# Optimization experiments

Measured on AMD Instinct MI355X. Metric: run time of the kernel, lower is better.

The kernel has to match this reference:

```python
import jax, jax.numpy as jnp
import numpy as np

N_USER, N_ITEM = 60000, 60000
N = N_USER + N_ITEM
E_BASE = 1500000
P = 200000
IN_DIM, HID, OUT = 128, 128, 64
K_MAX = 0.5


def setup_inputs() -> dict:
    key = jax.random.key(0)
    ks = jax.random.split(key, 20)
    feat_user = jax.random.normal(ks[0], (N_USER, 256), jnp.float32)
    feat_item = jax.random.normal(ks[1], (N_ITEM, 128), jnp.float32)
    src_b = jax.random.randint(ks[2], (E_BASE,), 0, N, jnp.int32)
    dst_b = jax.random.randint(ks[3], (E_BASE,), 0, N, jnp.int32)
    loops = jnp.arange(N, dtype=jnp.int32)  # dgl.add_self_loop
    src = jnp.concatenate([src_b, loops])
    dst = jnp.concatenate([dst_b, loops])
    pos_src = jax.random.randint(ks[4], (P,), 0, N, jnp.int32)
    pos_dst = jax.random.randint(ks[5], (P,), 0, N, jnp.int32)
    neg_src = jax.random.randint(ks[6], (P,), 0, N, jnp.int32)
    neg_dst = jax.random.randint(ks[7], (P,), 0, N, jnp.int32)
    s = 0.05
    W_user = jax.random.normal(ks[8], (256, IN_DIM), jnp.float32) * s
    b_user = jnp.zeros((IN_DIM,), jnp.float32)
    W_item = jax.random.normal(ks[9], (128, IN_DIM), jnp.float32) * s
    b_item = jnp.zeros((IN_DIM,), jnp.float32)
    W_gat = jax.random.normal(ks[10], (IN_DIM, HID), jnp.float32) * s
    attn_l = jax.random.normal(ks[11], (HID,), jnp.float32) * s
    attn_r = jax.random.normal(ks[12], (HID,), jnp.float32) * s
    gat_bias = jnp.zeros((HID,), jnp.float32)
    W_pred = jax.random.normal(ks[13], (HID, OUT), jnp.float32) * s
    b_pred = jnp.zeros((OUT,), jnp.float32)
    return {
        "feat_user": feat_user, "feat_item": feat_item,
        "W_user": W_user, "b_user": b_user, "W_item": W_item, "b_item": b_item,
        "W_gat": W_gat, "attn_l": attn_l, "attn_r": attn_r, "gat_bias": gat_bias,
        "W_pred": W_pred, "b_pred": b_pred,
        "src": src, "dst": dst,
        "pos_src": pos_src, "pos_dst": pos_dst,
        "neg_src": neg_src, "neg_dst": neg_dst,
        "alpha_T": 1,
    }


def _gat_conv(x, src, dst, W_gat, attn_l, attn_r, gat_bias):
    # DGL GATConv, 1 head: fc (no bias), additive attention, edge softmax over dst.
    z = x @ W_gat                              # [N, HID]
    el = z @ attn_l                            # [N]
    er = z @ attn_r                            # [N]
    e = jax.nn.leaky_relu(el[src] + er[dst], 0.2)   # [E]
    m = jax.ops.segment_max(e, dst, num_segments=N)  # per-dst max (self loops -> no empty segs)
    ex = jnp.exp(e - m[dst])
    ssum = jax.ops.segment_sum(ex, dst, num_segments=N)
    a = ex / ssum[dst]                          # edge softmax coeffs
    msg = z[src] * a[:, None]                   # [E, HID]
    out = jax.ops.segment_sum(msg, dst, num_segments=N) + gat_bias
    return jax.nn.elu(out)                      # activation=F.elu


def _hold_loss(score, k_T):
    l = jax.nn.log_sigmoid(score)
    hold = k_T * jnp.max(l)
    l = jnp.where(l > hold, 0.0, l)
    return -jnp.sum(l)


def reference(feat_user, feat_item, W_user, b_user, W_item, b_item,
              W_gat, attn_l, attn_r, gat_bias, W_pred, b_pred,
              src, dst, pos_src, pos_dst, neg_src, neg_dst, alpha_T):
    # per-type input projection then concat in ntype order (dgl.to_homogeneous)
    hu = feat_user @ W_user + b_user
    hi = feat_item @ W_item + b_item
    x = jnp.concatenate([hu, hi], axis=0)       # [N, IN_DIM]
    h = _gat_conv(x, src, dst, W_gat, attn_l, attn_r, gat_bias)
    pos_score = jnp.sum(h[pos_src] * h[pos_dst], axis=1)
    neg_score = jnp.sum(h[neg_src] * h[neg_dst], axis=1)
    k_T = K_MAX if K_MAX <= alpha_T else alpha_T   # k_T = min(k_max, alpha_T)
    loss = _hold_loss(pos_score, k_T) + _hold_loss(neg_score, k_T)
    out = h[:N_USER] @ W_pred + b_pred          # predict_type 'user' == type id 0
    return loss, out
```

## Files before the change

### kernel.cpp

```cpp
#include <hip/hip_runtime.h>
#include <hip/hip_bf16.h>
#include <math.h>

#define NUSER 60000
#define NITEM 60000
#define NNODE 120000
#define BSH 9
#define NB 235
#define CAP 8192

typedef __attribute__((ext_vector_type(8))) short bf16x8;
typedef __attribute__((ext_vector_type(4))) float f32x4;
typedef __attribute__((ext_vector_type(2))) float f32x2;
typedef __attribute__((ext_vector_type(4))) unsigned short u16x4;

__device__ __forceinline__ float leaky02(float x) { return x > 0.f ? x : 0.2f * x; }

__device__ __forceinline__ float inv_ord(unsigned int u) {
  unsigned int bits = (u & 0x80000000u) ? (u & 0x7FFFFFFFu) : ~u;
  return __uint_as_float(bits);
}
__device__ __forceinline__ unsigned int ord_of(float f) {
  unsigned int u = __float_as_uint(f);
  return (u & 0x80000000u) ? ~u : (u | 0x80000000u);
}
__device__ __forceinline__ short f2bs(float f) {
  __hip_bfloat16 h = __float2bfloat16(f);
  return *reinterpret_cast<short*>(&h);
}

__device__ __forceinline__ void f8fma(f32x2& acc, float w, unsigned int u) {
  f32x2 zz = __builtin_amdgcn_cvt_pk_f32_fp8(u, false);
  f32x2 ww; ww.x = w; ww.y = w;
  acc = __builtin_elementwise_fma(ww, zz, acc);
}
__device__ __forceinline__ void fp8dot(f32x2& acc, unsigned int ua, unsigned int ub) {
  f32x2 a0 = __builtin_amdgcn_cvt_pk_f32_fp8(ua, false);
  f32x2 a1 = __builtin_amdgcn_cvt_pk_f32_fp8(ua, true);
  f32x2 b0 = __builtin_amdgcn_cvt_pk_f32_fp8(ub, false);
  f32x2 b1 = __builtin_amdgcn_cvt_pk_f32_fp8(ub, true);
  acc = __builtin_elementwise_fma(a0, b0, acc);
  acc = __builtin_elementwise_fma(a1, b1, acc);
}

__global__ __launch_bounds__(256) void prep_count_kernel(
    const float* __restrict__ Wu, const float* __restrict__ bu, const float* __restrict__ Wi,
    const float* __restrict__ bi, const float* __restrict__ Wg, const float* __restrict__ Wp,
    __hip_bfloat16* __restrict__ Bp_u, __hip_bfloat16* __restrict__ Bp_i,
    __hip_bfloat16* __restrict__ Bp_p, float* __restrict__ bf_u, float* __restrict__ bf_i,
    const int* __restrict__ dst, int* __restrict__ btotal, int E) {
  __shared__ int cnt[NB];
  if (blockIdx.x < 512) {
    int bid = blockIdx.x;
    for (int t = threadIdx.x; t < NB; t += 256) cnt[t] = 0;
    __syncthreads();
    for (int i = bid * 256 + threadIdx.x; i < E; i += 512 * 256)
      atomicAdd(&cnt[dst[i] >> BSH], 1);
    __syncthreads();
    for (int t = threadIdx.x; t < NB; t += 256)
      if (cnt[t]) atomicAdd(&btotal[t], cnt[t]);
    return;
  }
  int t = (blockIdx.x - 512) * 256 + threadIdx.x;
  if (t < 32768) {
    int j = t & 7, lane = (t >> 3) & 63, rest = t >> 9;
    int nt = rest & 7, ks = rest >> 3;
    int k = ks * 32 + ((lane >> 4) << 3) + j;
    int n = nt * 16 + (lane & 15);
    float acc = 0.f;
#pragma unroll 8
    for (int jj = 0; jj < 128; ++jj) acc = fmaf(Wu[k * 128 + jj], Wg[jj * 128 + n], acc);
    Bp_u[t] = __float2bfloat16(acc);
  } else if (t < 49152) {
    int tt = t - 32768;
    int j = tt & 7, lane = (tt >> 3) & 63, rest = tt >> 9;
    int nt = rest & 7, ks = rest >> 3;
    int k = ks * 32 + ((lane >> 4) << 3) + j;
    int n = nt * 16 + (lane & 15);
    float acc = 0.f;
#pragma unroll 8
    for (int jj = 0; jj < 128; ++jj) acc = fmaf(Wi[k * 128 + jj], Wg[jj * 128 + n], acc);
    Bp_i[tt] = __float2bfloat16(acc);
  } else if (t < 57344) {
    int tt = t - 49152;
    int j = tt & 7, lane = (tt >> 3) & 63, rest = tt >> 9;
    int nt = rest & 3, ks = rest >> 2;
    int k = ks * 32 + ((lane >> 4) << 3) + j;
    int n = nt * 16 + (lane & 15);
    Bp_p[tt] = __float2bfloat16(Wp[k * 64 + n]);
  } else if (t < 57344 + 256) {
    int n = t - 57344;
    if (n < 128) {
      float acc = 0.f;
      for (int jj = 0; jj < 128; ++jj) acc = fmaf(bu[jj], Wg[jj * 128 + n], acc);
      bf_u[n] = acc;
    } else {
      int nn = n - 128;
      float acc = 0.f;
      for (int jj = 0; jj < 128; ++jj) acc = fmaf(bi[jj], Wg[jj * 128 + nn], acc);
      bf_i[nn] = acc;
    }
  }
}

__global__ void bscan_kernel(const int* __restrict__ btotal, int* __restrict__ bstart,
                             int* __restrict__ gcur) {
  __shared__ int s[256];
  int t = threadIdx.x;
  int v = (t < NB) ? btotal[t] : 0;
  s[t] = v;
  __syncthreads();
  for (int off = 1; off < 256; off <<= 1) {
    int a = (t >= off) ? s[t - off] : 0;
    __syncthreads();
    s[t] += a;
    __syncthreads();
  }
  int excl = s[t] - v;
  if (t < NB) { bstart[t] = excl; gcur[t] = excl; }
  if (t == NB - 1) bstart[NB] = s[t];
}

template <int K>
__device__ __forceinline__ void zgemm_body(
    char* smem, const float* __restrict__ A, const __hip_bfloat16* __restrict__ Bp,
    const float* __restrict__ bias, const float* __restrict__ al, const float* __restrict__ ar,
    unsigned char* __restrict__ z8, float* __restrict__ el, float* __restrict__ er, int M,
    int blk) {
  float(*lds)[140] = (float(*)[140])smem;
  const int lane = threadIdx.x & 63, wv = threadIdx.x >> 6;
  const int t = threadIdx.x;
  const int C4 = K / 4;
  for (int f = t; f < 64 * C4; f += 256) {
    int row = f / C4, c4 = f - row * C4;
    int grow = blk * 64 + row;
    if (grow >= M) grow = M - 1;
    float4 a = *(const float4*)(A + (size_t)grow * K + c4 * 4);
    u16x4 pk;
    pk[0] = (unsigned short)f2bs(a.x);
    pk[1] = (unsigned short)f2bs(a.y);
    pk[2] = (unsigned short)f2bs(a.z);
    pk[3] = (unsigned short)f2bs(a.w);
    unsigned int byte = (unsigned int)row * (K * 2) + (unsigned int)c4 * 8;
    byte ^= (row & 7) << 4;
    *(u16x4*)(smem + byte) = pk;
  }
  __syncthreads();
  const bf16x8* bp = (const bf16x8*)Bp;
  const int frow = wv * 16 + (lane & 15);
  f32x4 acc[8] = {};
#pragma unroll
  for (int ks = 0; ks < K / 32; ++ks) {
    unsigned int byte = (unsigned int)frow * (K * 2) + (unsigned int)(ks * 32 + ((lane >> 4) << 3)) * 2;
    byte ^= (frow & 7) << 4;
    bf16x8 af = *(const bf16x8*)(smem + byte);
#pragma unroll
    for (int nt = 0; nt < 8; ++nt) {
      bf16x8 bfr = bp[(ks * 8 + nt) * 64 + lane];
      acc[nt] = __builtin_amdgcn_mfma_f32_16x16x32_bf16(af, bfr, acc[nt], 0, 0, 0);
    }
  }
  __syncthreads();
#pragma unroll
  for (int nt = 0; nt < 8; ++nt) {
    float b = bias[nt * 16 + (lane & 15)];
#pragma unroll
    for (int r = 0; r < 4; ++r)
      lds[wv * 16 + (lane >> 4) * 4 + r][nt * 16 + (lane & 15)] = acc[nt][r] + b;
  }
  __syncthreads();
  int row = threadIdx.x >> 2;
  int q = threadIdx.x & 3;
  int gm = blk * 64 + row;
  float pl = 0.f, pr = 0.f;
  if (gm < M) {
    const float* lrow = &lds[row][q * 32];
#pragma unroll
    for (int v4 = 0; v4 < 4; ++v4) {
      float f[8];
#pragma unroll
      for (int j = 0; j < 8; ++j) {
        f[j] = lrow[v4 * 8 + j];
        int c = q * 32 + v4 * 8 + j;
        pl = fmaf(f[j], al[c], pl);
        pr = fmaf(f[j], ar[c], pr);
      }
      unsigned int w0 = (unsigned int)__builtin_amdgcn_cvt_pk_fp8_f32(f[0], f[1], 0, false);
      w0 = (unsigned int)__builtin_amdgcn_cvt_pk_fp8_f32(f[2], f[3], (int)w0, true);
      unsigned int w1 = (unsigned int)__builtin_amdgcn_cvt_pk_fp8_f32(f[4], f[5], 0, false);
      w1 = (unsigned int)__builtin_amdgcn_cvt_pk_fp8_f32(f[6], f[7], (int)w1, true);
      uint2 st; st.x = w0; st.y = w1;
      *(uint2*)(z8 + (size_t)gm * 128 + q * 32 + v4 * 8) = st;
    }
  }
  pl += __shfl_xor(pl, 1, 64); pl += __shfl_xor(pl, 2, 64);
  pr += __shfl_xor(pr, 1, 64); pr += __shfl_xor(pr, 2, 64);
  if (q == 0 && gm < M) { el[gm] = pl; er[gm] = pr; }
}

__global__ __launch_bounds__(256) void zgemm_scatter_kernel(
    const float* __restrict__ Au, const __hip_bfloat16* __restrict__ Bpu,
    const float* __restrict__ bfu, const float* __restrict__ Ai,
    const __hip_bfloat16* __restrict__ Bpi, const float* __restrict__ bfi,
    const float* __restrict__ al, const float* __restrict__ ar, unsigned char* __restrict__ z8,
    float* __restrict__ el, float* __restrict__ er, int SC, int GU,
    const int* __restrict__ src, const int* __restrict__ dst, int* __restrict__ gcur,
    unsigned int* __restrict__ scratch, int E) {
  __shared__ __align__(16) char smem[64 * 140 * 4];
  int bx = blockIdx.x;
  if (bx < SC) {
    int* cnt = (int*)smem;
    int* basep = cnt + NB;
    for (int t = threadIdx.x; t < NB; t += 256) cnt[t] = 0;
    __syncthreads();
    const int i0 = bx * 4096;
    unsigned int v_[16];
    int b_[16], r_[16];
#pragma unroll
    for (int j = 0; j < 16; ++j) {
      int i = i0 + j * 256 + threadIdx.x;
      b_[j] = -1;
      if (i < E) {
        int d = dst[i];
        int s = src[i];
        int b = d >> BSH;
        b_[j] = b;
        r_[j] = atomicAdd(&cnt[b], 1);
        v_[j] = (unsigned int)s | ((unsigned int)(d & 511) << 17);
      }
    }
    __syncthreads();
    for (int t = threadIdx.x; t < NB; t += 256)
      basep[t] = cnt[t] ? atomicAdd(&gcur[t], cnt[t]) : 0;
    __syncthreads();
#pragma unroll
    for (int j = 0; j < 16; ++j)
      if (b_[j] >= 0) scratch[basep[b_[j]] + r_[j]] = v_[j];
    return;
  }
  int gb = bx - SC;
  if (gb < GU)
    zgemm_body<256>(smem, Au, Bpu, bfu, al, ar, z8, el, er, NUSER, gb);
  else
    zgemm_body<128>(smem, Ai, Bpi, bfi, al, ar, z8 + (size_t)NUSER * 128, el + NUSER, er + NUSER,
                    NITEM, gb - GU);
}

__global__ __launch_bounds__(512) void bsort_kernel(const unsigned int* __restrict__ scratch,
                                                    const int* __restrict__ bstart,
                                                    int* __restrict__ offs, int* __restrict__ ssrc) {
  __shared__ unsigned int buf[CAP];
  __shared__ int cnt[512], scn[512], cur[512];
  int b = blockIdx.x, t = threadIdx.x;
  int s = bstart[b], e = bstart[b + 1], n = e - s;
  int d0 = b << BSH;
  int ndst = NNODE - d0;
  if (ndst > 512) ndst = 512;
  cnt[t] = 0;
  cur[t] = 0;
  __syncthreads();
  bool fit = (n <= CAP);
  if (fit) {
    for (int i = t; i < n; i += 512) {
      unsigned int v = scratch[s + i];
      buf[i] = v;
      atomicAdd(&cnt[v >> 17], 1);
    }
  } else {
    for (int i = t; i < n; i += 512) atomicAdd(&cnt[scratch[s + i] >> 17], 1);
  }
  __syncthreads();
  scn[t] = cnt[t];
  __syncthreads();
  for (int off = 1; off < 512; off <<= 1) {
    int a = (t >= off) ? scn[t - off] : 0;
    __syncthreads();
    scn[t] += a;
    __syncthreads();
  }
  int start = scn[t] - cnt[t];
  if (t < ndst) offs[d0 + t] = s + start;
  if (b == NB - 1 && t == 0) offs[NNODE] = e;
  __syncthreads();
  cnt[t] = start;
  __syncthreads();
  if (fit) {
    for (int i = t; i < n; i += 512) {
      unsigned int v = buf[i];
      int dl = v >> 17;
      int r = atomicAdd(&cur[dl], 1);
      ssrc[s + cnt[dl] + r] = (int)(v & 0x1FFFFu);
    }
  } else {
    for (int i = t; i < n; i += 512) {
      unsigned int v = scratch[s + i];
      int dl = v >> 17;
      int r = atomicAdd(&cur[dl], 1);
      ssrc[s + cnt[dl] + r] = (int)(v & 0x1FFFFu);
    }
  }
}

__global__ __launch_bounds__(256) void aggregate_kernel(
    const unsigned char* __restrict__ z8, const float* __restrict__ el,
    const float* __restrict__ er, const int* __restrict__ offs, const int* __restrict__ ssrc,
    const float* __restrict__ gat_bias, __hip_bfloat16* __restrict__ h,
    unsigned char* __restrict__ h8) {
  __shared__ __align__(16) float2 ew[4][128];
  int wv = threadIdx.x >> 6, lane = threadIdx.x & 63;
  int d = blockIdx.x * 4 + wv;
  int s0 = offs[d], s1 = offs[d + 1];
  int deg = s1 - s0;
  float erd = er[d];
  const unsigned short* zw = (const unsigned short*)z8;
  f32x2 acc = {0.f, 0.f};
  float ssum = 0.f;
  if (deg <= 128) {
    float w0 = 0.f, w1 = 0.f;
    int o0 = 0, o1 = 0;
    if (lane < deg) { int s = ssrc[s0 + lane]; o0 = s << 6; w0 = __expf(leaky02(el[s] + erd)); }
    if (64 + lane < deg) { int s = ssrc[s0 + 64 + lane]; o1 = s << 6; w1 = __expf(leaky02(el[s] + erd)); }
    ew[wv][lane] = make_float2(w0, __int_as_float(o0));
    ew[wv][64 + lane] = make_float2(w1, __int_as_float(o1));
    __builtin_amdgcn_wave_barrier();
    int i = 0;
    for (; i + 8 <= deg; i += 8) {
      float4 p0 = *(const float4*)&ew[wv][i];
      float4 p1 = *(const float4*)&ew[wv][i + 2];
      float4 p2 = *(const float4*)&ew[wv][i + 4];
      float4 p3 = *(const float4*)&ew[wv][i + 6];
      unsigned int u0 = zw[__float_as_uint(p0.y) + lane];
      unsigned int u1 = zw[__float_as_uint(p0.w) + lane];
      unsigned int u2 = zw[__float_as_uint(p1.y) + lane];
      unsigned int u3 = zw[__float_as_uint(p1.w) + lane];
      unsigned int u4 = zw[__float_as_uint(p2.y) + lane];
      unsigned int u5 = zw[__float_as_uint(p2.w) + lane];
      unsigned int u6 = zw[__float_as_uint(p3.y) + lane];
      unsigned int u7 = zw[__float_as_uint(p3.w) + lane];
      ssum += ((p0.x + p0.z) + (p1.x + p1.z)) + ((p2.x + p2.z) + (p3.x + p3.z));
      f8fma(acc, p0.x, u0); f8fma(acc, p0.z, u1);
      f8fma(acc, p1.x, u2); f8fma(acc, p1.z, u3);
      f8fma(acc, p2.x, u4); f8fma(acc, p2.z, u5);
      f8fma(acc, p3.x, u6); f8fma(acc, p3.z, u7);
    }
    for (; i + 2 <= deg; i += 2) {
      float4 p = *(const float4*)&ew[wv][i];
      unsigned int ua = zw[__float_as_uint(p.y) + lane];
      unsigned int ub = zw[__float_as_uint(p.w) + lane];
      ssum += p.x + p.z;
      f8fma(acc, p.x, ua); f8fma(acc, p.z, ub);
    }
    if (i < deg) {
      float2 pp = ew[wv][i];
      unsigned int u = zw[__float_as_uint(pp.y) + lane];
      ssum += pp.x;
      f8fma(acc, pp.x, u);
    }
  } else {
    for (int i2 = s0; i2 < s1; ++i2) {
      int s = ssrc[i2];
      float w = __expf(leaky02(el[s] + erd));
      ssum += w;
      unsigned int u = zw[((unsigned int)s << 6) + lane];
      f8fma(acc, w, u);
    }
  }
  float inv = 1.f / ssum;
  float o0f = acc.x * inv + gat_bias[lane * 2];
  float o1f = acc.y * inv + gat_bias[lane * 2 + 1];
  o0f = (o0f > 0.f) ? o0f : (__expf(o0f) - 1.f);
  o1f = (o1f > 0.f) ? o1f : (__expf(o1f) - 1.f);
  ushort2 ov;
  ov.x = (unsigned short)((unsigned int)f2bs(o0f) & 0xFFFFu);
  ov.y = (unsigned short)((unsigned int)f2bs(o1f) & 0xFFFFu);
  *(ushort2*)((unsigned short*)h + (size_t)d * 128 + lane * 2) = ov;
  int pk8 = __builtin_amdgcn_cvt_pk_fp8_f32(o0f, o1f, 0, false);
  *(unsigned short*)(h8 + (size_t)d * 128 + lane * 2) = (unsigned short)(pk8 & 0xFFFF);
}

__global__ __launch_bounds__(256) void scorepred_kernel(
    const unsigned char* __restrict__ h8, const int* __restrict__ ps, const int* __restrict__ pd,
    const int* __restrict__ ns, const int* __restrict__ nd, float* __restrict__ l_pos,
    float* __restrict__ l_neg, unsigned int* __restrict__ maxacc, int P,
    const __hip_bfloat16* __restrict__ h, const __hip_bfloat16* __restrict__ Bp,
    const float* __restrict__ bias, float* __restrict__ outp, int GP, int NSB) {
  if ((int)blockIdx.x < GP) {
    const int lane = threadIdx.x & 63, wv = threadIdx.x >> 6;
    const int m0 = blockIdx.x * 64 + wv * 16;
    int arow = m0 + (lane & 15);
    if (arow >= NUSER) arow = NUSER - 1;
    const bf16x8* a0 = (const bf16x8*)(h + (size_t)arow * 128) + (lane >> 4);
    const bf16x8* bp = (const bf16x8*)Bp;
    f32x4 acc[4] = {};
#pragma unroll
    for (int ks = 0; ks < 4; ++ks) {
      bf16x8 af = a0[ks * 4];
#pragma unroll
      for (int nt = 0; nt < 4; ++nt) {
        bf16x8 bfr = bp[(ks * 4 + nt) * 64 + lane];
        acc[nt] = __builtin_amdgcn_mfma_f32_16x16x32_bf16(af, bfr, acc[nt], 0, 0, 0);
      }
    }
#pragma unroll
    for (int nt = 0; nt < 4; ++nt) {
      int col = nt * 16 + (lane & 15);
      float b = bias[col];
#pragma unroll
      for (int r = 0; r < 4; ++r) {
        int m = m0 + (lane >> 4) * 4 + r;
        if (m < NUSER) outp[(size_t)m * 64 + col] = acc[nt][r] + b;
      }
    }
    return;
  }
  const int sb = blockIdx.x - GP;
  const int g16 = threadIdx.x >> 4, l16 = threadIdx.x & 15;
  const uint2* h2 = (const uint2*)h8;
  const int stride = NSB * 16;
  const int tot = 2 * P;
  float mpos = -1e30f, mneg = -1e30f;

  int i = sb * 16 + g16;
  int aC = 0, bC = 0;
  if (i < tot) {
    bool n = i >= P; int j = n ? i - P : i;
    aC = n ? ns[j] : ps[j]; bC = n ? nd[j] : pd[j];
  }
  uint2 vaC = {0, 0}, vbC = {0, 0};
  if (i < tot) {
    vaC = h2[(size_t)aC * 16 + l16];
    vbC = h2[(size_t)bC * 16 + l16];
  }
  int i1 = i + stride;
  int aN = 0, bN = 0;
  if (i1 < tot) {
    bool n = i1 >= P; int j = n ? i1 - P : i1;
    aN = n ? ns[j] : ps[j]; bN = n ? nd[j] : pd[j];
  }

  while (i < tot) {
    uint2 vaN = {0, 0}, vbN = {0, 0};
    if (i1 < tot) {
      vaN = h2[(size_t)aN * 16 + l16];
      vbN = h2[(size_t)bN * 16 + l16];
    }
    int i2 = i1 + stride;
    int aN2 = 0, bN2 = 0;
    if (i2 < tot) {
      bool n = i2 >= P; int j = n ? i2 - P : i2;
      aN2 = n ? ns[j] : ps[j]; bN2 = n ? nd[j] : pd[j];
    }
    f32x2 acc = {0.f, 0.f};
    fp8dot(acc, vaC.x, vbC.x);
    fp8dot(acc, vaC.y, vbC.y);
    float s = acc.x + acc.y;
    s += __shfl_xor(s, 1, 16);
    s += __shfl_xor(s, 2, 16);
    s += __shfl_xor(s, 4, 16);
    s += __shfl_xor(s, 8, 16);
    float lv = fminf(s, 0.f) - log1pf(__expf(-fabsf(s)));
    bool neg = i >= P;
    int j = neg ? i - P : i;
    if (l16 == 0) (neg ? l_neg : l_pos)[j] = lv;
    if (neg) mneg = fmaxf(mneg, lv); else mpos = fmaxf(mpos, lv);
    i = i1; i1 = i2;
    aC = aN; bC = bN; aN = aN2; bN = bN2;
    vaC = vaN; vbC = vbN;
  }
  __shared__ float red0[256], red1[256];
  red0[threadIdx.x] = mpos;
  red1[threadIdx.x] = mneg;
  __syncthreads();
  for (int off = 128; off; off >>= 1) {
    if (threadIdx.x < off) {
      red0[threadIdx.x] = fmaxf(red0[threadIdx.x], red0[threadIdx.x + off]);
      red1[threadIdx.x] = fmaxf(red1[threadIdx.x], red1[threadIdx.x + off]);
    }
    __syncthreads();
  }
  if (threadIdx.x == 0) {
    atomicMax(maxacc + 0, ord_of(red0[0]));
    atomicMax(maxacc + 1, ord_of(red1[0]));
  }
}

__global__ __launch_bounds__(256) void loss_sum_kernel(const float* __restrict__ l_pos,
                                                       const float* __restrict__ l_neg,
                                                       const unsigned int* __restrict__ maxacc,
                                                       const int* __restrict__ alpha,
                                                       float* __restrict__ sums,
                                                       unsigned int* __restrict__ fincnt,
                                                       float* __restrict__ out, int P) {
  __shared__ float sdata[256];
  int which = blockIdx.x >> 9;
  const float* l = which ? l_neg : l_pos;
  float a = (float)alpha[0];
  float kT = (0.5f <= a) ? 0.5f : a;
  float hold = kT * inv_ord(maxacc[which]);
  float s = 0.f;
  for (int i = (blockIdx.x & 511) * 256 + threadIdx.x; i < P; i += 512 * 256) {
    float v = l[i];
    if (!(v > hold)) s += v;
  }
  sdata[threadIdx.x] = s;
  __syncthreads();
  for (int off = 128; off; off >>= 1) {
    if (threadIdx.x < off) sdata[threadIdx.x] += sdata[threadIdx.x + off];
    __syncthreads();
  }
  if (threadIdx.x == 0) {
    atomicAdd(&sums[which], sdata[0]);
    __threadfence();
    unsigned int t = atomicAdd(fincnt, 1u);
    if (t == 1023u) {
      float s0 = atomicAdd(&sums[0], 0.f);
      float s1 = atomicAdd(&sums[1], 0.f);
      out[0] = -(s0 + s1);
    }
  }
}

extern "C" void kernel_launch(void* const* d_in, const int* in_sizes, int n_in,
                              void* d_out, int out_size, void* d_ws, size_t ws_size,
                              hipStream_t stream) {
  const float* feat_user = (const float*)d_in[0];
  const float* feat_item = (const float*)d_in[1];
  const float* W_user = (const float*)d_in[2];
  const float* b_user = (const float*)d_in[3];
  const float* W_item = (const float*)d_in[4];
  const float* b_item = (const float*)d_in[5];
  const float* W_gat = (const float*)d_in[6];
  const float* attn_l = (const float*)d_in[7];
  const float* attn_r = (const float*)d_in[8];
  const float* gat_bias = (const float*)d_in[9];
  const float* W_pred = (const float*)d_in[10];
  const float* b_pred = (const float*)d_in[11];
  const int* src = (const int*)d_in[12];
  const int* dst = (const int*)d_in[13];
  const int* pos_src = (const int*)d_in[14];
  const int* pos_dst = (const int*)d_in[15];
  const int* neg_src = (const int*)d_in[16];
  const int* neg_dst = (const int*)d_in[17];
  const int* alpha = (const int*)d_in[18];
  const int E = in_sizes[12];
  const int P = in_sizes[14];

  char* p = (char*)d_ws;
  auto alloc = [&](size_t bytes) {
    char* r = p;
    p += (bytes + 255) & ~(size_t)255;
    return r;
  };
  unsigned char* z8 = (unsigned char*)alloc((size_t)NNODE * 128);
  __hip_bfloat16* h = (__hip_bfloat16*)alloc((size_t)NNODE * 128 * 2);
  unsigned char* h8 = (unsigned char*)alloc((size_t)NNODE * 128);
  float* el = (float*)alloc((size_t)NNODE * 4);
  float* er = (float*)alloc((size_t)NNODE * 4);
  __hip_bfloat16* Bp_u = (__hip_bfloat16*)alloc(256 * 128 * 2);
  __hip_bfloat16* Bp_i = (__hip_bfloat16*)alloc(128 * 128 * 2);
  __hip_bfloat16* Bp_p = (__hip_bfloat16*)alloc(128 * 64 * 2);
  float* bf_u = (float*)alloc(128 * 4);
  float* bf_i = (float*)alloc(128 * 4);
  int* offs = (int*)alloc((size_t)(NNODE + 4) * 4);
  int* ssrc = (int*)alloc((size_t)E * 4);
  unsigned int* scratch = (unsigned int*)alloc((size_t)E * 4);
  float* l_pos = (float*)alloc((size_t)P * 4);
  float* l_neg = (float*)alloc((size_t)P * 4);
  int* bstart = (int*)alloc((NB + 1) * 4);
  int* gcur = (int*)alloc(NB * 4);
  int* btotal = (int*)alloc((NB + 8) * 4);
  unsigned int* maxacc = (unsigned int*)(btotal + NB);
  float* sums = (float*)(maxacc + 2);
  unsigned int* fincnt = (unsigned int*)(sums + 2);

  hipMemsetAsync(btotal, 0, (NB + 8) * 4, stream);

  prep_count_kernel<<<512 + 225, 256, 0, stream>>>(W_user, b_user, W_item, b_item, W_gat, W_pred,
                                                   Bp_u, Bp_i, Bp_p, bf_u, bf_i, dst, btotal, E);
  bscan_kernel<<<1, 256, 0, stream>>>(btotal, bstart, gcur);
  const int GU = (NUSER + 63) / 64, GI = (NITEM + 63) / 64;
  const int SC = (E + 4095) / 4096;
  zgemm_scatter_kernel<<<SC + GU + GI, 256, 0, stream>>>(feat_user, Bp_u, bf_u, feat_item, Bp_i,
                                                         bf_i, attn_l, attn_r, z8, el, er, SC, GU,
                                                         src, dst, gcur, scratch, E);
  bsort_kernel<<<NB, 512, 0, stream>>>(scratch, bstart, offs, ssrc);
  aggregate_kernel<<<NNODE / 4, 256, 0, stream>>>(z8, el, er, offs, ssrc, gat_bias, h, h8);
  const int GP = (NUSER + 63) / 64;
  const int NSB = 2048;
  scorepred_kernel<<<GP + NSB, 256, 0, stream>>>(h8, pos_src, pos_dst, neg_src, neg_dst, l_pos,
                                                 l_neg, maxacc, P, h, Bp_p, b_pred,
                                                 (float*)d_out + 1, GP, NSB);
  loss_sum_kernel<<<1024, 256, 0, stream>>>(l_pos, l_neg, maxacc, alpha, sums, fincnt,
                                            (float*)d_out, P);

  (void)n_in; (void)out_size; (void)ws_size;
}
```

Measured before the change: 247.1 us.

## Shrink zgemm LDS footprint via K-halving and split epilogue; widen pair-score loads

The zgemm body now stages A in 128-column chunks and writes the epilogue through a 64-column staging tile in two passes, so shared memory drops from about 35.8KB to 17.9KB per block. The aim is higher occupancy for the fused zgemm/scatter kernel, at the cost of extra barriers. Separately, the pos/neg scoring loop uses 8 lanes per pair with 16-byte loads instead of 16 lanes with 8-byte loads. That gives fewer shuffles per pair and more pairs in flight per block.

```diff
diff --git a/kernel.cpp b/kernel.cpp
--- a/kernel.cpp
+++ b/kernel.cpp
@@ -127,75 +127,81 @@
     const float* __restrict__ bias, const float* __restrict__ al, const float* __restrict__ ar,
     unsigned char* __restrict__ z8, float* __restrict__ el, float* __restrict__ er, int M,
     int blk) {
-  float(*lds)[140] = (float(*)[140])smem;
   const int lane = threadIdx.x & 63, wv = threadIdx.x >> 6;
   const int t = threadIdx.x;
-  const int C4 = K / 4;
-  for (int f = t; f < 64 * C4; f += 256) {
-    int row = f / C4, c4 = f - row * C4;
-    int grow = blk * 64 + row;
-    if (grow >= M) grow = M - 1;
-    float4 a = *(const float4*)(A + (size_t)grow * K + c4 * 4);
-    u16x4 pk;
-    pk[0] = (unsigned short)f2bs(a.x);
-    pk[1] = (unsigned short)f2bs(a.y);
-    pk[2] = (unsigned short)f2bs(a.z);
-    pk[3] = (unsigned short)f2bs(a.w);
-    unsigned int byte = (unsigned int)row * (K * 2) + (unsigned int)c4 * 8;
-    byte ^= (row & 7) << 4;
-    *(u16x4*)(smem + byte) = pk;
-  }
-  __syncthreads();
   const bf16x8* bp = (const bf16x8*)Bp;
   const int frow = wv * 16 + (lane & 15);
   f32x4 acc[8] = {};
 #pragma unroll
-  for (int ks = 0; ks < K / 32; ++ks) {
-    unsigned int byte = (unsigned int)frow * (K * 2) + (unsigned int)(ks * 32 + ((lane >> 4) << 3)) * 2;
-    byte ^= (frow & 7) << 4;
-    bf16x8 af = *(const bf16x8*)(smem + byte);
-#pragma unroll
-    for (int nt = 0; nt < 8; ++nt) {
-      bf16x8 bfr = bp[(ks * 8 + nt) * 64 + lane];
-      acc[nt] = __builtin_amdgcn_mfma_f32_16x16x32_bf16(af, bfr, acc[nt], 0, 0, 0);
-    }
-  }
-  __syncthreads();
-#pragma unroll
-  for (int nt = 0; nt < 8; ++nt) {
-    float b = bias[nt * 16 + (lane & 15)];
-#pragma unroll
-    for (int r = 0; r < 4; ++r)
-      lds[wv * 16 + (lane >> 4) * 4 + r][nt * 16 + (lane & 15)] = acc[nt][r] + b;
-  }
-  __syncthreads();
-  int row = threadIdx.x >> 2;
-  int q = threadIdx.x & 3;
+  for (int half = 0; half < K / 128; ++half) {
+    for (int f = t; f < 64 * 32; f += 256) {
+      int row = f >> 5, c4 = f & 31;
+      int grow = blk * 64 + row;
+      if (grow >= M) grow = M - 1;
+      float4 a = *(const float4*)(A + (size_t)grow * K + half * 128 + c4 * 4);
+      u16x4 pk;
+      pk[0] = (unsigned short)f2bs(a.x);
+      pk[1] = (unsigned short)f2bs(a.y);
+      pk[2] = (unsigned short)f2bs(a.z);
+      pk[3] = (unsigned short)f2bs(a.w);
+      unsigned int byte = ((unsigned int)row << 8) + ((unsigned int)c4 << 3);
+      byte ^= (row & 7) << 4;
+      *(u16x4*)(smem + byte) = pk;
+    }
+    __syncthreads();
+#pragma unroll
+    for (int ks2 = 0; ks2 < 4; ++ks2) {
+      int ks = half * 4 + ks2;
+      unsigned int byte = ((unsigned int)frow << 8) +
+                          ((unsigned int)(ks2 * 32 + ((lane >> 4) << 3)) << 1);
+      byte ^= (frow & 7) << 4;
+      bf16x8 af = *(const bf16x8*)(smem + byte);
+#pragma unroll
+      for (int nt = 0; nt < 8; ++nt) {
+        bf16x8 bfr = bp[(ks * 8 + nt) * 64 + lane];
+        acc[nt] = __builtin_amdgcn_mfma_f32_16x16x32_bf16(af, bfr, acc[nt], 0, 0, 0);
+      }
+    }
+    __syncthreads();
+  }
+  float(*lds2)[68] = (float(*)[68])smem;
+  int row = t >> 2, qq = t & 3;
   int gm = blk * 64 + row;
   float pl = 0.f, pr = 0.f;
-  if (gm < M) {
-    const float* lrow = &lds[row][q * 32];
-#pragma unroll
-    for (int v4 = 0; v4 < 4; ++v4) {
-      float f[8];
-#pragma unroll
-      for (int j = 0; j < 8; ++j) {
-        f[j] = lrow[v4 * 8 + j];
-        int c = q * 32 + v4 * 8 + j;
-        pl = fmaf(f[j], al[c], pl);
-        pr = fmaf(f[j], ar[c], pr);
+#pragma unroll
+  for (int p = 0; p < 2; ++p) {
+    __syncthreads();
+#pragma unroll
+    for (int nt = p * 4; nt < p * 4 + 4; ++nt) {
+      float b = bias[nt * 16 + (lane & 15)];
+#pragma unroll
+      for (int r = 0; r < 4; ++r)
+        lds2[wv * 16 + (lane >> 4) * 4 + r][(nt & 3) * 16 + (lane & 15)] = acc[nt][r] + b;
+    }
+    __syncthreads();
+    if (gm < M) {
+#pragma unroll
+      for (int v4 = 0; v4 < 2; ++v4) {
+        float f[8];
+#pragma unroll
+        for (int j = 0; j < 8; ++j) {
+          f[j] = lds2[row][qq * 16 + v4 * 8 + j];
+          int c = p * 64 + qq * 16 + v4 * 8 + j;
+          pl = fmaf(f[j], al[c], pl);
+          pr = fmaf(f[j], ar[c], pr);
+        }
+        unsigned int w0 = (unsigned int)__builtin_amdgcn_cvt_pk_fp8_f32(f[0], f[1], 0, false);
+        w0 = (unsigned int)__builtin_amdgcn_cvt_pk_fp8_f32(f[2], f[3], (int)w0, true);
+        unsigned int w1 = (unsigned int)__builtin_amdgcn_cvt_pk_fp8_f32(f[4], f[5], 0, false);
+        w1 = (unsigned int)__builtin_amdgcn_cvt_pk_fp8_f32(f[6], f[7], (int)w1, true);
+        uint2 st; st.x = w0; st.y = w1;
+        *(uint2*)(z8 + (size_t)gm * 128 + p * 64 + qq * 16 + v4 * 8) = st;
       }
-      unsigned int w0 = (unsigned int)__builtin_amdgcn_cvt_pk_fp8_f32(f[0], f[1], 0, false);
-      w0 = (unsigned int)__builtin_amdgcn_cvt_pk_fp8_f32(f[2], f[3], (int)w0, true);
-      unsigned int w1 = (unsigned int)__builtin_amdgcn_cvt_pk_fp8_f32(f[4], f[5], 0, false);
-      w1 = (unsigned int)__builtin_amdgcn_cvt_pk_fp8_f32(f[6], f[7], (int)w1, true);
-      uint2 st; st.x = w0; st.y = w1;
-      *(uint2*)(z8 + (size_t)gm * 128 + q * 32 + v4 * 8) = st;
     }
   }
   pl += __shfl_xor(pl, 1, 64); pl += __shfl_xor(pl, 2, 64);
   pr += __shfl_xor(pr, 1, 64); pr += __shfl_xor(pr, 2, 64);
-  if (q == 0 && gm < M) { el[gm] = pl; er[gm] = pr; }
+  if (qq == 0 && gm < M) { el[gm] = pl; er[gm] = pr; }
 }
 
 __global__ __launch_bounds__(256) void zgemm_scatter_kernel(
@@ -206,7 +212,7 @@
     float* __restrict__ el, float* __restrict__ er, int SC, int GU,
     const int* __restrict__ src, const int* __restrict__ dst, int* __restrict__ gcur,
     unsigned int* __restrict__ scratch, int E) {
-  __shared__ __align__(16) char smem[64 * 140 * 4];
+  __shared__ __align__(16) char smem[17920];
   int bx = blockIdx.x;
   if (bx < SC) {
     int* cnt = (int*)smem;
@@ -414,22 +420,22 @@
     return;
   }
   const int sb = blockIdx.x - GP;
-  const int g16 = threadIdx.x >> 4, l16 = threadIdx.x & 15;
-  const uint2* h2 = (const uint2*)h8;
-  const int stride = NSB * 16;
+  const int g8 = threadIdx.x >> 3, l8 = threadIdx.x & 7;
+  const uint4* h4 = (const uint4*)h8;
+  const int stride = NSB * 32;
   const int tot = 2 * P;
   float mpos = -1e30f, mneg = -1e30f;
 
-  int i = sb * 16 + g16;
+  int i = sb * 32 + g8;
   int aC = 0, bC = 0;
   if (i < tot) {
     bool n = i >= P; int j = n ? i - P : i;
     aC = n ? ns[j] : ps[j]; bC = n ? nd[j] : pd[j];
   }
-  uint2 vaC = {0, 0}, vbC = {0, 0};
+  uint4 vaC = {0, 0, 0, 0}, vbC = {0, 0, 0, 0};
   if (i < tot) {
-    vaC = h2[(size_t)aC * 16 + l16];
-    vbC = h2[(size_t)bC * 16 + l16];
+    vaC = h4[(size_t)aC * 8 + l8];
+    vbC = h4[(size_t)bC * 8 + l8];
   }
   int i1 = i + stride;
   int aN = 0, bN = 0;
@@ -439,10 +445,10 @@
   }
 
   while (i < tot) {
-    uint2 vaN = {0, 0}, vbN = {0, 0};
+    uint4 vaN = {0, 0, 0, 0}, vbN = {0, 0, 0, 0};
     if (i1 < tot) {
-      vaN = h2[(size_t)aN * 16 + l16];
-      vbN = h2[(size_t)bN * 16 + l16];
+      vaN = h4[(size_t)aN * 8 + l8];
+      vbN = h4[(size_t)bN * 8 + l8];
     }
     int i2 = i1 + stride;
     int aN2 = 0, bN2 = 0;
@@ -453,15 +459,16 @@
     f32x2 acc = {0.f, 0.f};
     fp8dot(acc, vaC.x, vbC.x);
     fp8dot(acc, vaC.y, vbC.y);
+    fp8dot(acc, vaC.z, vbC.z);
+    fp8dot(acc, vaC.w, vbC.w);
     float s = acc.x + acc.y;
-    s += __shfl_xor(s, 1, 16);
-    s += __shfl_xor(s, 2, 16);
-    s += __shfl_xor(s, 4, 16);
-    s += __shfl_xor(s, 8, 16);
+    s += __shfl_xor(s, 1, 8);
+    s += __shfl_xor(s, 2, 8);
+    s += __shfl_xor(s, 4, 8);
     float lv = fminf(s, 0.f) - log1pf(__expf(-fabsf(s)));
     bool neg = i >= P;
     int j = neg ? i - P : i;
-    if (l16 == 0) (neg ? l_neg : l_pos)[j] = lv;
+    if (l8 == 0) (neg ? l_neg : l_pos)[j] = lv;
     if (neg) mneg = fmaxf(mneg, lv); else mpos = fmaxf(mpos, lv);
     i = i1; i1 = i2;
     aC = aN; bC = bN; aN = aN2; bN = bN2;
```

Measured after the change: 242.6 us. No clear change (-1.8%).
